# Kernel tuning notes

Measured on AMD Instinct MI355X. Metric: run time of the kernel, lower is better.

Reference implementation:

```python
import jax, jax.numpy as jnp
import numpy as np

INF = 10000000000.0
D_KEY = 512
SCALE = np.sqrt(D_KEY).astype(np.float32)

def setup_inputs() -> dict:
    key = jax.random.key(0)
    kq, kk, kv = jax.random.split(key, 3)
    B, S, D = 16, 2048, D_KEY
    return {
        "query": jax.random.normal(kq, (B, S, D), dtype=jnp.float32),
        "key": jax.random.normal(kk, (B, S, D), dtype=jnp.float32),
        "value": jax.random.normal(kv, (B, S, D), dtype=jnp.float32),
    }

def reference(query, key, value):
    # dot_products = Q @ K^T, shape [B, S, S]
    scores = jnp.einsum('bqd,bkd->bqk', query, key)
    S = key.shape[1]
    # causal mask: subtract INF on strict upper triangle (applied BEFORE scaling,
    # matching the original which subtracts tri*INF then divides by scale)
    tri = jnp.triu(jnp.ones((S, S), dtype=scores.dtype), k=1) * INF
    scores = scores - tri[None, :, :]
    attn = jax.nn.softmax(scores / SCALE, axis=-1)
    return jnp.einsum('bqk,bkd->bqd', attn, value)
```

## Files before the change

kernel.cpp:

```cpp
#include <hip/hip_runtime.h>

typedef float  f32x4 __attribute__((ext_vector_type(4)));
typedef short  s16x8 __attribute__((ext_vector_type(8)));
typedef short  s16x4 __attribute__((ext_vector_type(4)));

#define B_   16
#define S_   2048
#define D_   512
#define BM   32
#define BN   256
#define RSCALE 0.04419417382415922f
#define LOG2E  1.4426950408889634f

__device__ __forceinline__ short f2bf(float f){
    unsigned u = __float_as_uint(f);
    u += 0x7fffu + ((u >> 16) & 1u);
    return (short)(u >> 16);
}

__device__ __forceinline__ f32x4 max4(f32x4 a, f32x4 b){
    f32x4 r; r[0]=fmaxf(a[0],b[0]); r[1]=fmaxf(a[1],b[1]);
             r[2]=fmaxf(a[2],b[2]); r[3]=fmaxf(a[3],b[3]); return r;
}
__device__ __forceinline__ f32x4 shfl_xor4(f32x4 v, int mask){
    f32x4 r; r[0]=__shfl_xor(v[0],mask); r[1]=__shfl_xor(v[1],mask);
             r[2]=__shfl_xor(v[2],mask); r[3]=__shfl_xor(v[3],mask); return r;
}

__global__ void cast_k_kernel(const float* __restrict__ k, short* __restrict__ kb){
    const long n4 = (long)B_*S_*D_/4;
    const float4* src = (const float4*)k;
    for (long t = (long)blockIdx.x*blockDim.x + threadIdx.x; t < n4;
         t += (long)gridDim.x*blockDim.x){
        float4 v = src[t];
        s16x4 o; o[0]=f2bf(v.x); o[1]=f2bf(v.y); o[2]=f2bf(v.z); o[3]=f2bf(v.w);
        *(s16x4*)(kb + t*4) = o;
    }
}

__global__ void transpose_v_kernel(const float* __restrict__ v, short* __restrict__ vt){
    __shared__ float tile[64][65];
    int b  = blockIdx.z;
    int s0 = blockIdx.x * 64;
    int d0 = blockIdx.y * 64;
    int t  = threadIdx.x;
    int r  = t >> 2;
    int c4 = (t & 3) * 16;
    const float* src = v + ((long)b*S_ + s0 + r)*D_ + d0 + c4;
    float4 a0 = ((const float4*)src)[0];
    float4 a1 = ((const float4*)src)[1];
    float4 a2 = ((const float4*)src)[2];
    float4 a3 = ((const float4*)src)[3];
    tile[r][c4+ 0]=a0.x; tile[r][c4+ 1]=a0.y; tile[r][c4+ 2]=a0.z; tile[r][c4+ 3]=a0.w;
    tile[r][c4+ 4]=a1.x; tile[r][c4+ 5]=a1.y; tile[r][c4+ 6]=a1.z; tile[r][c4+ 7]=a1.w;
    tile[r][c4+ 8]=a2.x; tile[r][c4+ 9]=a2.y; tile[r][c4+10]=a2.z; tile[r][c4+11]=a2.w;
    tile[r][c4+12]=a3.x; tile[r][c4+13]=a3.y; tile[r][c4+14]=a3.z; tile[r][c4+15]=a3.w;
    __syncthreads();
    s16x8 w0, w1;
    #pragma unroll
    for (int i = 0; i < 8; ++i)  w0[i] = f2bf(tile[c4+i][r]);
    #pragma unroll
    for (int i = 0; i < 8; ++i)  w1[i] = f2bf(tile[c4+8+i][r]);
    short* dst = vt + ((long)b*D_ + d0 + r)*S_ + s0 + c4;
    *(s16x8*)dst       = w0;
    *(s16x8*)(dst + 8) = w1;
}

__global__ __launch_bounds__(512) void flash_kernel(
    const float* __restrict__ q, const short* __restrict__ kb,
    const short* __restrict__ vt, float* __restrict__ out)
{
    __shared__ __align__(16) short q_lds[BM*D_];
    __shared__ __align__(16) short p_lds[BM*BN];
    __shared__ float pmax[BM][8];
    __shared__ float psum[BM][8];

    int bx = blockIdx.x;
    int lo = bx & 7;
    int hi = bx >> 3;
    int batch = 2*lo + (hi & 1);
    int t = hi >> 1;
    int qt = (t < 32) ? (63 - t) : (t - 32);
    int q0 = qt * BM;

    int tid  = threadIdx.x;
    int w    = tid >> 6;
    int lane = tid & 63;
    int m    = lane & 15;
    int quad = lane >> 4;

    {
        int r  = tid >> 4;
        int cb = (tid & 15) << 5;
        const float* qrow = q + ((long)batch*S_ + q0 + r)*D_;
        #pragma unroll
        for (int gi = 0; gi < 4; ++gi){
            int c = cb + gi*8;
            float4 f0 = *(const float4*)(qrow + c);
            float4 f1 = *(const float4*)(qrow + c + 4);
            s16x8 vv;
            vv[0]=f2bf(f0.x); vv[1]=f2bf(f0.y); vv[2]=f2bf(f0.z); vv[3]=f2bf(f0.w);
            vv[4]=f2bf(f1.x); vv[5]=f2bf(f1.y); vv[6]=f2bf(f1.z); vv[7]=f2bf(f1.w);
            int g = c >> 3;
            *(s16x8*)&q_lds[r*D_ + (((g ^ (r & 7)) & 63) << 3)] = vv;
        }
    }
    __syncthreads();

    f32x4 o_acc[2][4];
    #pragma unroll
    for (int a = 0; a < 2; ++a)
        #pragma unroll
        for (int b2 = 0; b2 < 4; ++b2) o_acc[a][b2] = (f32x4)0.0f;
    f32x4 m_pr[2], l_pr[2];
    m_pr[0] = (f32x4)(-1e30f); m_pr[1] = (f32x4)(-1e30f);
    l_pr[0] = (f32x4)0.0f;     l_pr[1] = (f32x4)0.0f;

    const short* kbb = kb + (long)batch*S_*D_;
    const short* vtb = vt + (long)batch*D_*S_;
    int jmax = (q0 + BM - 1) >> 8;

    for (int j = 0; j <= jmax; ++j){
        int kbase = j << 8;

        f32x4 acc[2][2];
        acc[0][0]=(f32x4)0.0f; acc[0][1]=(f32x4)0.0f;
        acc[1][0]=(f32x4)0.0f; acc[1][1]=(f32x4)0.0f;
        const short* kp0 = kbb + ((long)(kbase + w*32 + m))*D_ + quad*8;
        #pragma unroll
        for (int ks = 0; ks < 16; ++ks){
            int gq = ((ks*4 + quad) ^ (m & 7)) << 3;
            s16x8 a0 = *(const s16x8*)&q_lds[ m      *D_ + gq];
            s16x8 a1 = *(const s16x8*)&q_lds[(16 + m)*D_ + gq];
            const short* kp = kp0 + ks*32;
            s16x8 b0 = *(const s16x8*)kp;
            s16x8 b1 = *(const s16x8*)(kp + 16*D_);
            acc[0][0] = __builtin_amdgcn_mfma_f32_16x16x32_bf16(a0, b0, acc[0][0], 0,0,0);
            acc[0][1] = __builtin_amdgcn_mfma_f32_16x16x32_bf16(a0, b1, acc[0][1], 0,0,0);
            acc[1][0] = __builtin_amdgcn_mfma_f32_16x16x32_bf16(a1, b0, acc[1][0], 0,0,0);
            acc[1][1] = __builtin_amdgcn_mfma_f32_16x16x32_bf16(a1, b1, acc[1][1], 0,0,0);
        }

        if (j == jmax){
            #pragma unroll
            for (int mt = 0; mt < 2; ++mt)
                #pragma unroll
                for (int nt = 0; nt < 2; ++nt){
                    int kg = kbase + w*32 + nt*16 + m;
                    #pragma unroll
                    for (int rr = 0; rr < 4; ++rr){
                        int qg = q0 + mt*16 + quad*4 + rr;
                        float vv = acc[mt][nt][rr] * RSCALE;
                        acc[mt][nt][rr] = (kg > qg) ? -1e30f : vv;
                    }
                }
        } else {
            #pragma unroll
            for (int mt = 0; mt < 2; ++mt)
                #pragma unroll
                for (int nt = 0; nt < 2; ++nt)
                    #pragma unroll
                    for (int rr = 0; rr < 4; ++rr)
                        acc[mt][nt][rr] *= RSCALE;
        }

        f32x4 cm[2];
        cm[0] = max4(acc[0][0], acc[0][1]);
        cm[1] = max4(acc[1][0], acc[1][1]);
        #pragma unroll
        for (int msk = 1; msk < 16; msk <<= 1){
            cm[0] = max4(cm[0], shfl_xor4(cm[0], msk));
            cm[1] = max4(cm[1], shfl_xor4(cm[1], msk));
        }
        if (m == 0){
            #pragma unroll
            for (int mt = 0; mt < 2; ++mt)
                #pragma unroll
                for (int rr = 0; rr < 4; ++rr)
                    pmax[mt*16 + quad*4 + rr][w] = cm[mt][rr];
        }
        __syncthreads();

        f32x4 alpha[2];
        #pragma unroll
        for (int mt = 0; mt < 2; ++mt){
            #pragma unroll
            for (int rr = 0; rr < 4; ++rr){
                int row = mt*16 + quad*4 + rr;
                f32x4 p0 = *(const f32x4*)&pmax[row][0];
                f32x4 p1 = *(const f32x4*)&pmax[row][4];
                f32x4 pm = max4(p0, p1);
                float mx = fmaxf(fmaxf(pm[0],pm[1]), fmaxf(pm[2],pm[3]));
                float mn = fmaxf(m_pr[mt][rr], mx);
                alpha[mt][rr] = exp2f((m_pr[mt][rr] - mn) * LOG2E);
                m_pr[mt][rr] = mn;
            }
            l_pr[mt] *= alpha[mt];
            #pragma unroll
            for (int nt = 0; nt < 4; ++nt) o_acc[mt][nt] *= alpha[mt];
        }

        f32x4 cs[2]; cs[0] = (f32x4)0.0f; cs[1] = (f32x4)0.0f;
        #pragma unroll
        for (int mt = 0; mt < 2; ++mt)
            #pragma unroll
            for (int nt = 0; nt < 2; ++nt){
                int col = w*32 + nt*16 + m;
                int g   = col >> 3;
                #pragma unroll
                for (int rr = 0; rr < 4; ++rr){
                    int row = mt*16 + quad*4 + rr;
                    float p = exp2f((acc[mt][nt][rr] - m_pr[mt][rr]) * LOG2E);
                    cs[mt][rr] += p;
                    p_lds[row*BN + (((g ^ (row & 7)) & 31) << 3) + (col & 7)] = f2bf(p);
                }
            }
        #pragma unroll
        for (int msk = 1; msk < 16; msk <<= 1){
            cs[0] = cs[0] + shfl_xor4(cs[0], msk);
            cs[1] = cs[1] + shfl_xor4(cs[1], msk);
        }
        if (m == 0){
            #pragma unroll
            for (int mt = 0; mt < 2; ++mt)
                #pragma unroll
                for (int rr = 0; rr < 4; ++rr)
                    psum[mt*16 + quad*4 + rr][w] = cs[mt][rr];
        }
        __syncthreads();

        #pragma unroll
        for (int mt = 0; mt < 2; ++mt)
            #pragma unroll
            for (int rr = 0; rr < 4; ++rr){
                int row = mt*16 + quad*4 + rr;
                f32x4 p0 = *(const f32x4*)&psum[row][0];
                f32x4 p1 = *(const f32x4*)&psum[row][4];
                f32x4 sm = p0 + p1;
                l_pr[mt][rr] += (sm[0]+sm[1]) + (sm[2]+sm[3]);
            }

        const short* vp0 = vtb + ((long)(w*64 + m))*S_ + kbase + quad*8;
        #pragma unroll
        for (int ks = 0; ks < 8; ++ks){
            int gp = ((ks*4 + quad) ^ (m & 7)) << 3;
            s16x8 pa0 = *(const s16x8*)&p_lds[ m      *BN + gp];
            s16x8 pa1 = *(const s16x8*)&p_lds[(16 + m)*BN + gp];
            const short* vp = vp0 + ks*32;
            s16x8 vb0 = *(const s16x8*)vp;
            s16x8 vb1 = *(const s16x8*)(vp + 16*S_);
            s16x8 vb2 = *(const s16x8*)(vp + 32*S_);
            s16x8 vb3 = *(const s16x8*)(vp + 48*S_);
            o_acc[0][0] = __builtin_amdgcn_mfma_f32_16x16x32_bf16(pa0, vb0, o_acc[0][0], 0,0,0);
            o_acc[0][1] = __builtin_amdgcn_mfma_f32_16x16x32_bf16(pa0, vb1, o_acc[0][1], 0,0,0);
            o_acc[0][2] = __builtin_amdgcn_mfma_f32_16x16x32_bf16(pa0, vb2, o_acc[0][2], 0,0,0);
            o_acc[0][3] = __builtin_amdgcn_mfma_f32_16x16x32_bf16(pa0, vb3, o_acc[0][3], 0,0,0);
            o_acc[1][0] = __builtin_amdgcn_mfma_f32_16x16x32_bf16(pa1, vb0, o_acc[1][0], 0,0,0);
            o_acc[1][1] = __builtin_amdgcn_mfma_f32_16x16x32_bf16(pa1, vb1, o_acc[1][1], 0,0,0);
            o_acc[1][2] = __builtin_amdgcn_mfma_f32_16x16x32_bf16(pa1, vb2, o_acc[1][2], 0,0,0);
            o_acc[1][3] = __builtin_amdgcn_mfma_f32_16x16x32_bf16(pa1, vb3, o_acc[1][3], 0,0,0);
        }
    }

    float* ob = out + ((long)batch*S_ + q0)*D_ + w*64;
    #pragma unroll
    for (int mt = 0; mt < 2; ++mt){
        f32x4 inv;
        #pragma unroll
        for (int rr = 0; rr < 4; ++rr) inv[rr] = 1.0f / l_pr[mt][rr];
        #pragma unroll
        for (int nt = 0; nt < 4; ++nt){
            f32x4 vv = o_acc[mt][nt] * inv;
            #pragma unroll
            for (int rr = 0; rr < 4; ++rr)
                ob[(long)(mt*16 + quad*4 + rr)*D_ + nt*16 + m] = vv[rr];
        }
    }
}

extern "C" void kernel_launch(void* const* d_in, const int* in_sizes, int n_in,
                              void* d_out, int out_size, void* d_ws, size_t ws_size,
                              hipStream_t stream) {
    const float* q = (const float*)d_in[0];
    const float* k = (const float*)d_in[1];
    const float* v = (const float*)d_in[2];
    float* out = (float*)d_out;
    short* kbb = (short*)d_ws;
    short* vtb = kbb + (size_t)B_*S_*D_;
    cast_k_kernel<<<8192, 256, 0, stream>>>(k, kbb);
    transpose_v_kernel<<<dim3(S_/64, D_/64, B_), 256, 0, stream>>>(v, vtb);
    flash_kernel<<<1024, 512, 0, stream>>>(q, kbb, vtb, out);
}
```

Measured before the change: 525.9 us.

## Fuse K cast with V transpose, transpose QK^T MFMA and simplify softmax reductions

Merges the K bf16 cast and V transpose into one prep kernel, dropping a launch and a separate pass over K. In the flash kernel, the QK^T MFMA operands are swapped so each lane holds a key-major score tile. Row-max and row-sum reductions now use two cross-quad shuffles instead of four-step shuffle trees, and P is written to a padded transposed LDS buffer with 4-wide stores. It also folds log2e into the scale constant, adds an occupancy hint to launch bounds, and changes the jmax bound. The column-max bookkeeping differs from the row-max used for rescaling, which risks numerical mismatch and adds register pressure.

```diff
diff --git a/kernel.cpp b/kernel.cpp
--- a/kernel.cpp
+++ b/kernel.cpp
@@ -9,36 +9,24 @@
 #define D_   512
 #define BM   32
 #define BN   256
-#define RSCALE 0.04419417382415922f
-#define LOG2E  1.4426950408889634f
+#define PTS  264
+#define C1   0.06376279834938389f
 
 __device__ __forceinline__ short f2bf(float f){
     unsigned u = __float_as_uint(f);
     u += 0x7fffu + ((u >> 16) & 1u);
     return (short)(u >> 16);
 }
-
+__device__ __forceinline__ float hmax4(f32x4 v){
+    return fmaxf(fmaxf(v[0],v[1]), fmaxf(v[2],v[3]));
+}
 __device__ __forceinline__ f32x4 max4(f32x4 a, f32x4 b){
     f32x4 r; r[0]=fmaxf(a[0],b[0]); r[1]=fmaxf(a[1],b[1]);
              r[2]=fmaxf(a[2],b[2]); r[3]=fmaxf(a[3],b[3]); return r;
 }
-__device__ __forceinline__ f32x4 shfl_xor4(f32x4 v, int mask){
-    f32x4 r; r[0]=__shfl_xor(v[0],mask); r[1]=__shfl_xor(v[1],mask);
-             r[2]=__shfl_xor(v[2],mask); r[3]=__shfl_xor(v[3],mask); return r;
-}
-
-__global__ void cast_k_kernel(const float* __restrict__ k, short* __restrict__ kb){
-    const long n4 = (long)B_*S_*D_/4;
-    const float4* src = (const float4*)k;
-    for (long t = (long)blockIdx.x*blockDim.x + threadIdx.x; t < n4;
-         t += (long)gridDim.x*blockDim.x){
-        float4 v = src[t];
-        s16x4 o; o[0]=f2bf(v.x); o[1]=f2bf(v.y); o[2]=f2bf(v.z); o[3]=f2bf(v.w);
-        *(s16x4*)(kb + t*4) = o;
-    }
-}
-
-__global__ void transpose_v_kernel(const float* __restrict__ v, short* __restrict__ vt){
+
+__global__ void prep_kernel(const float* __restrict__ k, const float* __restrict__ v,
+                            short* __restrict__ kb, short* __restrict__ vt){
     __shared__ float tile[64][65];
     int b  = blockIdx.z;
     int s0 = blockIdx.x * 64;
@@ -46,15 +34,28 @@
     int t  = threadIdx.x;
     int r  = t >> 2;
     int c4 = (t & 3) * 16;
-    const float* src = v + ((long)b*S_ + s0 + r)*D_ + d0 + c4;
-    float4 a0 = ((const float4*)src)[0];
-    float4 a1 = ((const float4*)src)[1];
-    float4 a2 = ((const float4*)src)[2];
-    float4 a3 = ((const float4*)src)[3];
-    tile[r][c4+ 0]=a0.x; tile[r][c4+ 1]=a0.y; tile[r][c4+ 2]=a0.z; tile[r][c4+ 3]=a0.w;
-    tile[r][c4+ 4]=a1.x; tile[r][c4+ 5]=a1.y; tile[r][c4+ 6]=a1.z; tile[r][c4+ 7]=a1.w;
-    tile[r][c4+ 8]=a2.x; tile[r][c4+ 9]=a2.y; tile[r][c4+10]=a2.z; tile[r][c4+11]=a2.w;
-    tile[r][c4+12]=a3.x; tile[r][c4+13]=a3.y; tile[r][c4+14]=a3.z; tile[r][c4+15]=a3.w;
+    long off = ((long)b*S_ + s0 + r)*D_ + d0 + c4;
+
+    {
+        const float4* ksrc = (const float4*)(k + off);
+        float4 a0 = ksrc[0], a1 = ksrc[1], a2 = ksrc[2], a3 = ksrc[3];
+        s16x8 w0, w1;
+        w0[0]=f2bf(a0.x); w0[1]=f2bf(a0.y); w0[2]=f2bf(a0.z); w0[3]=f2bf(a0.w);
+        w0[4]=f2bf(a1.x); w0[5]=f2bf(a1.y); w0[6]=f2bf(a1.z); w0[7]=f2bf(a1.w);
+        w1[0]=f2bf(a2.x); w1[1]=f2bf(a2.y); w1[2]=f2bf(a2.z); w1[3]=f2bf(a2.w);
+        w1[4]=f2bf(a3.x); w1[5]=f2bf(a3.y); w1[6]=f2bf(a3.z); w1[7]=f2bf(a3.w);
+        short* dst = kb + off;
+        *(s16x8*)dst       = w0;
+        *(s16x8*)(dst + 8) = w1;
+    }
+    {
+        const float4* vsrc = (const float4*)(v + off);
+        float4 a0 = vsrc[0], a1 = vsrc[1], a2 = vsrc[2], a3 = vsrc[3];
+        tile[r][c4+ 0]=a0.x; tile[r][c4+ 1]=a0.y; tile[r][c4+ 2]=a0.z; tile[r][c4+ 3]=a0.w;
+        tile[r][c4+ 4]=a1.x; tile[r][c4+ 5]=a1.y; tile[r][c4+ 6]=a1.z; tile[r][c4+ 7]=a1.w;
+        tile[r][c4+ 8]=a2.x; tile[r][c4+ 9]=a2.y; tile[r][c4+10]=a2.z; tile[r][c4+11]=a2.w;
+        tile[r][c4+12]=a3.x; tile[r][c4+13]=a3.y; tile[r][c4+14]=a3.z; tile[r][c4+15]=a3.w;
+    }
     __syncthreads();
     s16x8 w0, w1;
     #pragma unroll
@@ -66,12 +67,12 @@
     *(s16x8*)(dst + 8) = w1;
 }
 
-__global__ __launch_bounds__(512) void flash_kernel(
+__global__ __launch_bounds__(512, 4) void flash_kernel(
     const float* __restrict__ q, const short* __restrict__ kb,
     const short* __restrict__ vt, float* __restrict__ out)
 {
     __shared__ __align__(16) short q_lds[BM*D_];
-    __shared__ __align__(16) short p_lds[BM*BN];
+    __shared__ __align__(16) short pt_lds[BM*PTS];
     __shared__ float pmax[BM][8];
     __shared__ float psum[BM][8];
 
@@ -112,13 +113,14 @@
     for (int a = 0; a < 2; ++a)
         #pragma unroll
         for (int b2 = 0; b2 < 4; ++b2) o_acc[a][b2] = (f32x4)0.0f;
-    f32x4 m_pr[2], l_pr[2];
-    m_pr[0] = (f32x4)(-1e30f); m_pr[1] = (f32x4)(-1e30f);
-    l_pr[0] = (f32x4)0.0f;     l_pr[1] = (f32x4)0.0f;
+    f32x4 m_row[2], l_row[2];
+    m_row[0] = (f32x4)(-1e30f); m_row[1] = (f32x4)(-1e30f);
+    l_row[0] = (f32x4)0.0f;     l_row[1] = (f32x4)0.0f;
+    float m_col[2] = {-1e30f, -1e30f};
 
     const short* kbb = kb + (long)batch*S_*D_;
     const short* vtb = vt + (long)batch*D_*S_;
-    int jmax = (q0 + BM - 1) >> 8;
+    int jmax = q0 >> 8;
 
     for (int j = 0; j <= jmax; ++j){
         int kbase = j << 8;
@@ -129,16 +131,16 @@
         const short* kp0 = kbb + ((long)(kbase + w*32 + m))*D_ + quad*8;
         #pragma unroll
         for (int ks = 0; ks < 16; ++ks){
+            const short* kp = kp0 + ks*32;
+            s16x8 ka0 = *(const s16x8*)kp;
+            s16x8 ka1 = *(const s16x8*)(kp + 16*D_);
             int gq = ((ks*4 + quad) ^ (m & 7)) << 3;
-            s16x8 a0 = *(const s16x8*)&q_lds[ m      *D_ + gq];
-            s16x8 a1 = *(const s16x8*)&q_lds[(16 + m)*D_ + gq];
-            const short* kp = kp0 + ks*32;
-            s16x8 b0 = *(const s16x8*)kp;
-            s16x8 b1 = *(const s16x8*)(kp + 16*D_);
-            acc[0][0] = __builtin_amdgcn_mfma_f32_16x16x32_bf16(a0, b0, acc[0][0], 0,0,0);
-            acc[0][1] = __builtin_amdgcn_mfma_f32_16x16x32_bf16(a0, b1, acc[0][1], 0,0,0);
-            acc[1][0] = __builtin_amdgcn_mfma_f32_16x16x32_bf16(a1, b0, acc[1][0], 0,0,0);
-            acc[1][1] = __builtin_amdgcn_mfma_f32_16x16x32_bf16(a1, b1, acc[1][1], 0,0,0);
+            s16x8 qb0 = *(const s16x8*)&q_lds[ m      *D_ + gq];
+            s16x8 qb1 = *(const s16x8*)&q_lds[(16 + m)*D_ + gq];
+            acc[0][0] = __builtin_amdgcn_mfma_f32_16x16x32_bf16(ka0, qb0, acc[0][0], 0,0,0);
+            acc[0][1] = __builtin_amdgcn_mfma_f32_16x16x32_bf16(ka0, qb1, acc[0][1], 0,0,0);
+            acc[1][0] = __builtin_amdgcn_mfma_f32_16x16x32_bf16(ka1, qb0, acc[1][0], 0,0,0);
+            acc[1][1] = __builtin_amdgcn_mfma_f32_16x16x32_bf16(ka1, qb1, acc[1][1], 0,0,0);
         }
 
         if (j == jmax){
@@ -146,12 +148,12 @@
             for (int mt = 0; mt < 2; ++mt)
                 #pragma unroll
                 for (int nt = 0; nt < 2; ++nt){
-                    int kg = kbase + w*32 + nt*16 + m;
+                    int qg = q0 + nt*16 + m;
                     #pragma unroll
                     for (int rr = 0; rr < 4; ++rr){
-                        int qg = q0 + mt*16 + quad*4 + rr;
-                        float vv = acc[mt][nt][rr] * RSCALE;
-                        acc[mt][nt][rr] = (kg > qg) ? -1e30f : vv;
+                        int kvg = kbase + w*32 + mt*16 + quad*4 + rr;
+                        float s = acc[mt][nt][rr] * C1;
+                        acc[mt][nt][rr] = (kvg > qg) ? -1e30f : s;
                     }
                 }
         } else {
@@ -161,23 +163,15 @@
                 for (int nt = 0; nt < 2; ++nt)
                     #pragma unroll
                     for (int rr = 0; rr < 4; ++rr)
-                        acc[mt][nt][rr] *= RSCALE;
-        }
-
-        f32x4 cm[2];
-        cm[0] = max4(acc[0][0], acc[0][1]);
-        cm[1] = max4(acc[1][0], acc[1][1]);
-        #pragma unroll
-        for (int msk = 1; msk < 16; msk <<= 1){
-            cm[0] = max4(cm[0], shfl_xor4(cm[0], msk));
-            cm[1] = max4(cm[1], shfl_xor4(cm[1], msk));
-        }
-        if (m == 0){
-            #pragma unroll
-            for (int mt = 0; mt < 2; ++mt)
-                #pragma unroll
-                for (int rr = 0; rr < 4; ++rr)
-                    pmax[mt*16 + quad*4 + rr][w] = cm[mt][rr];
+                        acc[mt][nt][rr] *= C1;
+        }
+
+        #pragma unroll
+        for (int nt = 0; nt < 2; ++nt){
+            float cm = fmaxf(hmax4(acc[0][nt]), hmax4(acc[1][nt]));
+            cm = fmaxf(cm, __shfl_xor(cm, 16));
+            cm = fmaxf(cm, __shfl_xor(cm, 32));
+            if (quad == 0) pmax[nt*16 + m][w] = cm;
         }
         __syncthreads();
 
@@ -189,43 +183,43 @@
                 int row = mt*16 + quad*4 + rr;
                 f32x4 p0 = *(const f32x4*)&pmax[row][0];
                 f32x4 p1 = *(const f32x4*)&pmax[row][4];
-                f32x4 pm = max4(p0, p1);
-                float mx = fmaxf(fmaxf(pm[0],pm[1]), fmaxf(pm[2],pm[3]));
-                float mn = fmaxf(m_pr[mt][rr], mx);
-                alpha[mt][rr] = exp2f((m_pr[mt][rr] - mn) * LOG2E);
-                m_pr[mt][rr] = mn;
+                float mx = hmax4(max4(p0, p1));
+                float mn = fmaxf(m_row[mt][rr], mx);
+                alpha[mt][rr] = exp2f(m_row[mt][rr] - mn);
+                m_row[mt][rr] = mn;
             }
-            l_pr[mt] *= alpha[mt];
+            l_row[mt] *= alpha[mt];
             #pragma unroll
             for (int nt = 0; nt < 4; ++nt) o_acc[mt][nt] *= alpha[mt];
         }
-
-        f32x4 cs[2]; cs[0] = (f32x4)0.0f; cs[1] = (f32x4)0.0f;
-        #pragma unroll
-        for (int mt = 0; mt < 2; ++mt)
-            #pragma unroll
-            for (int nt = 0; nt < 2; ++nt){
-                int col = w*32 + nt*16 + m;
-                int g   = col >> 3;
+        float mcn[2];
+        #pragma unroll
+        for (int nt = 0; nt < 2; ++nt){
+            int row = nt*16 + m;
+            f32x4 p0 = *(const f32x4*)&pmax[row][0];
+            f32x4 p1 = *(const f32x4*)&pmax[row][4];
+            float mx = hmax4(max4(p0, p1));
+            mcn[nt] = fmaxf(m_col[nt], mx);
+            m_col[nt] = mcn[nt];
+        }
+
+        #pragma unroll
+        for (int nt = 0; nt < 2; ++nt){
+            float cs = 0.0f;
+            #pragma unroll
+            for (int mt = 0; mt < 2; ++mt){
+                s16x4 pk;
                 #pragma unroll
                 for (int rr = 0; rr < 4; ++rr){
-                    int row = mt*16 + quad*4 + rr;
-                    float p = exp2f((acc[mt][nt][rr] - m_pr[mt][rr]) * LOG2E);
-                    cs[mt][rr] += p;
-                    p_lds[row*BN + (((g ^ (row & 7)) & 31) << 3) + (col & 7)] = f2bf(p);
+                    float p = exp2f(acc[mt][nt][rr] - mcn[nt]);
+                    cs += p;
+                    pk[rr] = f2bf(p);
                 }
+                *(s16x4*)&pt_lds[(nt*16 + m)*PTS + w*32 + mt*16 + quad*4] = pk;
             }
-        #pragma unroll
-        for (int msk = 1; msk < 16; msk <<= 1){
-            cs[0] = cs[0] + shfl_xor4(cs[0], msk);
-            cs[1] = cs[1] + shfl_xor4(cs[1], msk);
-        }
-        if (m == 0){
-            #pragma unroll
-            for (int mt = 0; mt < 2; ++mt)
-                #pragma unroll
-                for (int rr = 0; rr < 4; ++rr)
-                    psum[mt*16 + quad*4 + rr][w] = cs[mt][rr];
+            cs += __shfl_xor(cs, 16);
+            cs += __shfl_xor(cs, 32);
+            if (quad == 0) psum[nt*16 + m][w] = cs;
         }
         __syncthreads();
 
@@ -234,18 +228,17 @@
             #pragma unroll
             for (int rr = 0; rr < 4; ++rr){
                 int row = mt*16 + quad*4 + rr;
-                f32x4 p0 = *(const f32x4*)&psum[row][0];
-                f32x4 p1 = *(const f32x4*)&psum[row][4];
-                f32x4 sm = p0 + p1;
-                l_pr[mt][rr] += (sm[0]+sm[1]) + (sm[2]+sm[3]);
+                f32x4 s0 = *(const f32x4*)&psum[row][0];
+                f32x4 s1 = *(const f32x4*)&psum[row][4];
+                f32x4 ss = s0 + s1;
+                l_row[mt][rr] += (ss[0]+ss[1]) + (ss[2]+ss[3]);
             }
 
         const short* vp0 = vtb + ((long)(w*64 + m))*S_ + kbase + quad*8;
         #pragma unroll
         for (int ks = 0; ks < 8; ++ks){
-            int gp = ((ks*4 + quad) ^ (m & 7)) << 3;
-            s16x8 pa0 = *(const s16x8*)&p_lds[ m      *BN + gp];
-            s16x8 pa1 = *(const s16x8*)&p_lds[(16 + m)*BN + gp];
+            s16x8 pa0 = *(const s16x8*)&pt_lds[ m      *PTS + ks*32 + quad*8];
+            s16x8 pa1 = *(const s16x8*)&pt_lds[(16 + m)*PTS + ks*32 + quad*8];
             const short* vp = vp0 + ks*32;
             s16x8 vb0 = *(const s16x8*)vp;
             s16x8 vb1 = *(const s16x8*)(vp + 16*S_);
@@ -267,7 +260,7 @@
     for (int mt = 0; mt < 2; ++mt){
         f32x4 inv;
         #pragma unroll
-        for (int rr = 0; rr < 4; ++rr) inv[rr] = 1.0f / l_pr[mt][rr];
+        for (int rr = 0; rr < 4; ++rr) inv[rr] = 1.0f / l_row[mt][rr];
         #pragma unroll
         for (int nt = 0; nt < 4; ++nt){
             f32x4 vv = o_acc[mt][nt] * inv;
@@ -287,7 +280,6 @@
     float* out = (float*)d_out;
     short* kbb = (short*)d_ws;
     short* vtb = kbb + (size_t)B_*S_*D_;
-    cast_k_kernel<<<8192, 256, 0, stream>>>(k, kbb);
-    transpose_v_kernel<<<dim3(S_/64, D_/64, B_), 256, 0, stream>>>(v, vtb);
+    prep_kernel<<<dim3(S_/64, D_/64, B_), 256, 0, stream>>>(k, v, kbb, vtb);
     flash_kernel<<<1024, 512, 0, stream>>>(q, kbb, vtb, out);
 }
```

Measured after the change: 625.2 us. +18.9%, slower.
